# Optimization experiments

Hardware: AMD Instinct MI355X
Metric: run time of the kernel (lower is better)

The kernel has to match this reference:

```python
import jax, jax.numpy as jnp
import numpy as np

EMBED, ACT, MEM, STOCH, HID = 256, 7, 200, 30, 200
MIN_STD = 0.1
T, B = 256, 512


def setup_inputs() -> dict:
    key = jax.random.key(0)
    ks = jax.random.split(key, 16)

    def w(k, shape, fan_in):
        return (jax.random.normal(k, shape, jnp.float32) / np.sqrt(fan_in)).astype(jnp.float32)

    inp = {
        "embed": jax.random.normal(ks[0], (T, B, EMBED), jnp.float32),
        "action": jax.random.normal(ks[1], (T, B, ACT), jnp.float32),
        "reset": jax.random.randint(ks[2], (T, B), 0, 2).astype(bool),
        "in_state": jnp.zeros((B, MEM), jnp.float32),
        "noise": jax.random.normal(ks[3], (B, STOCH), jnp.float32),
        # ea_mlp: Linear(embed+action -> hidden)
        "W_ea": w(ks[4], (EMBED + ACT, HID), EMBED + ACT),
        "b_ea": jnp.zeros((HID,), jnp.float32),
        # GRUCell(hidden -> mem): torch layout [3*mem] ordered (r, z, n)
        "W_ih": w(ks[5], (HID, 3 * MEM), HID),
        "b_ih": jnp.zeros((3 * MEM,), jnp.float32),
        "W_hh": w(ks[6], (MEM, 3 * MEM), MEM),
        "b_hh": jnp.zeros((3 * MEM,), jnp.float32),
        # post_mlp: Linear(mem->hidden), ELU, Linear(hidden->2*stoch)
        "Wp1": w(ks[7], (MEM, HID), MEM),
        "bp1": jnp.zeros((HID,), jnp.float32),
        "Wp2": w(ks[8], (HID, 2 * STOCH), HID),
        "bp2": jnp.zeros((2 * STOCH,), jnp.float32),
    }
    return inp


def reference(embed, action, reset, in_state, noise,
              W_ea, b_ea, W_ih, b_ih, W_hh, b_hh, Wp1, bp1, Wp2, bp2):
    def post_mlp(h):
        mid = jax.nn.elu(h @ Wp1 + bp1)
        return mid @ Wp2 + bp2

    def to_mean_std(x):
        mean, std = jnp.split(x, 2, axis=-1)
        return jnp.concatenate([mean, jax.nn.softplus(std) + MIN_STD], axis=-1)

    def step(h, xs):
        e, a, r = xs  # e:[B,EMBED] a:[B,ACT] r:[B] bool
        h = h * (~r)[:, None].astype(h.dtype)
        ea = jax.nn.elu(jnp.concatenate([e, a], axis=-1) @ W_ea + b_ea)
        gi = ea @ W_ih + b_ih  # [B, 3*MEM]
        gh = h @ W_hh + b_hh
        gi_r, gi_z, gi_n = jnp.split(gi, 3, axis=-1)
        gh_r, gh_z, gh_n = jnp.split(gh, 3, axis=-1)
        rg = jax.nn.sigmoid(gi_r + gh_r)
        zg = jax.nn.sigmoid(gi_z + gh_z)
        ng = jnp.tanh(gi_n + rg * gh_n)
        h_new = (1.0 - zg) * ng + zg * h  # torch GRUCell update
        post = to_mean_std(post_mlp(h_new))
        return h_new, (h_new, post)

    _, (states, posts) = jax.lax.scan(step, in_state, (embed, action, reset))
    mean, std = jnp.split(posts[-1], 2, axis=-1)
    sample = mean + std * noise  # rsample of diag Normal
    return sample, states, posts
```

## Files before the change

kernel.cpp:

```cpp
#include <hip/hip_runtime.h>
#include <math.h>

#define EMBED 256
#define ACTD  7
#define MEM   200
#define STOCH 30
#define T_    256
#define B_    512
#define EAIN  263
#define G3    600

typedef unsigned int uint32;
typedef _Float16 h2v   __attribute__((ext_vector_type(2)));
typedef _Float16 f16x8 __attribute__((ext_vector_type(8)));
typedef float    f32x4 __attribute__((ext_vector_type(4)));

__device__ __forceinline__ float eluf(float x)  { return x > 0.f ? x : expm1f(x); }
__device__ __forceinline__ float sigmf(float x) { return 1.f / (1.f + __expf(-x)); }
__device__ __forceinline__ float splusf(float x){ return fmaxf(x, 0.f) + log1pf(__expf(-fabsf(x))); }

__device__ __forceinline__ uint32 packh2(float a, float b) {
#if __has_builtin(__builtin_amdgcn_cvt_pkrtz)
    auto h = __builtin_amdgcn_cvt_pkrtz(a, b);
    return __builtin_bit_cast(uint32, h);
#else
    h2v h; h.x = (_Float16)a; h.y = (_Float16)b;
    return __builtin_bit_cast(uint32, h);
#endif
}

__global__ void detect_kernel(const unsigned char* __restrict__ p, int n, int* __restrict__ flags)
{
    __shared__ int s_mis, s_gt1;
    if (threadIdx.x == 0) { s_mis = 0; s_gt1 = 0; }
    __syncthreads();
    int mis = 0, gt1 = 0;
    for (int i = threadIdx.x; i < n; i += blockDim.x) {
        unsigned char v = p[i];
        if (v) {
            if (i & 3) mis = 1;
            if (v > 1) gt1 = 1;
        }
    }
    if (mis) atomicOr(&s_mis, 1);
    if (gt1) atomicOr(&s_gt1, 1);
    __syncthreads();
    if (threadIdx.x == 0) flags[0] = s_mis ? (s_gt1 ? 2 : 1) : 0;
}

__device__ __forceinline__ bool resetval(const unsigned char* __restrict__ p, int mode, int idx)
{
    if (mode == 0) return ((const int*)p)[idx] != 0;
    if (mode == 1) return p[idx] != 0;
    return ((const float*)p)[idx] != 0.f;
}

__global__ void packT_kernel(const float* __restrict__ src, uint32* __restrict__ dst,
                             int K, int C, int Cpad, int K2pad)
{
    int idx = blockIdx.x * blockDim.x + threadIdx.x;
    if (idx < Cpad * K2pad) {
        int c = idx / K2pad, k2 = idx % K2pad;
        float a = (c < C && 2 * k2     < K) ? src[(size_t)(2 * k2)     * C + c] : 0.f;
        float b = (c < C && 2 * k2 + 1 < K) ? src[(size_t)(2 * k2 + 1) * C + c] : 0.f;
        dst[idx] = packh2(a, b);
    }
}

#define GI3_T 512

__global__ __launch_bounds__(GI3_T)
void gi3_kernel(const float* __restrict__ embed, const float* __restrict__ action,
                const uint32* __restrict__ WeaT, const float* __restrict__ b_ea,
                const uint32* __restrict__ WihT, const float* __restrict__ b_ih,
                uint32* __restrict__ gi_pk, int row_base)
{
    __shared__ __align__(16) uint32 Epk[32 * 148];
    __shared__ __align__(16) uint32 eapk[32 * 116];

    const int tid = threadIdx.x, lane = tid & 63, wv = tid >> 6;
    const int lo = lane & 15, hi = lane >> 4, r0 = hi * 4;
    const int rel0 = blockIdx.x * 32;
    const int rg0  = row_base + rel0;

    for (int idx = tid; idx < 32 * 144; idx += GI3_T) {
        int r = idx / 144, k2 = idx % 144;
        size_t rg = (size_t)(rg0 + r);
        float a = 0.f, b = 0.f;
        if (k2 < 128) {
            const float2 v = *(const float2*)&embed[rg * EMBED + 2 * k2];
            a = v.x; b = v.y;
        } else if (k2 < 132) {
            int k = 2 * k2 - EMBED;
            a = action[rg * ACTD + k];
            b = (k + 1 < ACTD) ? action[rg * ACTD + k + 1] : 0.f;
        }
        Epk[r * 148 + k2] = packh2(a, b);
    }
    { int r = tid >> 4, o = tid & 15; eapk[r * 116 + 100 + o] = 0; }
    __syncthreads();

    const _Float16* E16  = (const _Float16*)Epk;
    _Float16*       ea16 = (_Float16*)eapk;

    f16x8 afr[2][9];
    #pragma unroll
    for (int mt = 0; mt < 2; mt++)
        #pragma unroll
        for (int kt = 0; kt < 9; kt++)
            afr[mt][kt] = *(const f16x8*)&E16[(mt * 16 + lo) * 296 + kt * 32 + hi * 8];

    for (int nt = wv; nt < 13; nt += 8) {
        int col = nt * 16 + lo;
        float bv = (col < 200) ? b_ea[col] : 0.f;
        f16x8 wb[9];
        #pragma unroll
        for (int kt = 0; kt < 9; kt++)
            wb[kt] = *(const f16x8*)&WeaT[col * 144 + kt * 16 + hi * 4];
        #pragma unroll
        for (int mt = 0; mt < 2; mt++) {
            f32x4 acc = {bv, bv, bv, bv};
            #pragma unroll
            for (int kt = 0; kt < 9; kt++)
                acc = __builtin_amdgcn_mfma_f32_16x16x32_f16(afr[mt][kt], wb[kt], acc, 0, 0, 0);
            #pragma unroll
            for (int j = 0; j < 4; j++)
                ea16[(mt * 16 + r0 + j) * 232 + col] = (_Float16)eluf(acc[j]);
        }
    }
    __syncthreads();

    f16x8 afr2[2][7];
    #pragma unroll
    for (int mt = 0; mt < 2; mt++)
        #pragma unroll
        for (int kt = 0; kt < 7; kt++)
            afr2[mt][kt] = *(const f16x8*)&ea16[(mt * 16 + lo) * 232 + kt * 32 + hi * 8];

    for (int nt = wv; nt < 38; nt += 8) {
        int col = nt * 16 + lo;
        float bv = (col < G3) ? b_ih[col] : 0.f;
        f16x8 wb[7];
        #pragma unroll
        for (int kt = 0; kt < 7; kt++)
            wb[kt] = *(const f16x8*)&WihT[col * 112 + kt * 16 + hi * 4];
        #pragma unroll
        for (int mt = 0; mt < 2; mt++) {
            f32x4 acc = {bv, bv, bv, bv};
            #pragma unroll
            for (int kt = 0; kt < 7; kt++)
                acc = __builtin_amdgcn_mfma_f32_16x16x32_f16(afr2[mt][kt], wb[kt], acc, 0, 0, 0);
            #pragma unroll
            for (int j = 0; j < 4; j++) {
                float v = acc[j];
                float p = __shfl_xor(v, 1);
                if (((lane & 1) == 0) && col < G3)
                    gi_pk[(size_t)(rel0 + mt * 16 + r0 + j) * 300 + (col >> 1)] = packh2(v, p);
            }
        }
    }
}

#define RR 8

__global__ __launch_bounds__(512, 2)
void recur5_kernel(const uint32* __restrict__ gi_pk, const uint32* __restrict__ WhhT,
                   const float* __restrict__ b_hh, const float* __restrict__ in_state,
                   const unsigned char* __restrict__ reset_raw, const int* __restrict__ flags,
                   float* __restrict__ out_states, float* __restrict__ h_buf,
                   int t0, int t1, int first)
{
    __shared__ _Float16 h_lds[16 * 232];
    __shared__ float    gh_lds[RR * 612];
    __shared__ float    rst_lds[RR];

    const int tid = threadIdx.x, lane = tid & 63, wv = tid >> 6;
    const int lo = lane & 15, hi = lane >> 4, r0c = hi * 4;
    const int bg0 = blockIdx.x * RR;
    const int mode = flags[0];
    uint32* h32 = (uint32*)h_lds;

    f16x8 bfr[5][7];
    float bcol[5];
    #pragma unroll
    for (int i = 0; i < 5; ++i) {
        int ct  = wv + 8 * i;
        int col = ct * 16 + lo;
        bcol[i] = (ct < 38 && col < G3) ? b_hh[col] : 0.f;
        #pragma unroll
        for (int kt = 0; kt < 7; ++kt)
            bfr[i][kt] = (ct < 38) ? *(const f16x8*)&WhhT[col * 112 + kt * 16 + hi * 4]
                                   : f16x8{0, 0, 0, 0, 0, 0, 0, 0};
    }

    for (int idx = tid; idx < 1056; idx += 512) {
        int r, o;
        if (idx < 128) { r = idx >> 4; o = 100 + (idx & 15); }
        else { int j = idx - 128; r = 8 + j / 116; o = j % 116; }
        h32[r * 116 + o] = 0;
    }

    float hold[2][2];
    #pragma unroll
    for (int it = 0; it < 2; ++it) {
        int u2 = it * 512 + tid;
        if (u2 < RR * 100) {
            int row = u2 / 100, mp = u2 % 100, m = mp * 2;
            float a, b;
            if (first) {
                const float2 v = *(const float2*)&in_state[(size_t)(bg0 + row) * MEM + m];
                a = v.x; b = v.y;
                if (resetval(reset_raw, mode, bg0 + row)) { a = 0.f; b = 0.f; }
            } else {
                const float2 v = *(const float2*)&h_buf[(size_t)(bg0 + row) * MEM + m];
                a = v.x; b = v.y;
            }
            hold[it][0] = a; hold[it][1] = b;
            h32[row * 116 + mp] = packh2(a, b);
        }
    }
    __syncthreads();

    uint32 pcur[2][3], pnxt[2][3];
    {
        const size_t base32 = (size_t)bg0 * 300;
        #pragma unroll
        for (int it = 0; it < 2; ++it) {
            int u2 = it * 512 + tid;
            if (u2 < RR * 100) {
                int row = u2 / 100, mp = u2 % 100;
                pcur[it][0] = gi_pk[base32 + row * 300 + mp];
                pcur[it][1] = gi_pk[base32 + row * 300 + 100 + mp];
                pcur[it][2] = gi_pk[base32 + row * 300 + 200 + mp];
            }
        }
    }

    for (int t = t0; t < t1; ++t) {
        if (t + 1 < t1) {
            const size_t base32 = ((size_t)(t + 1 - t0) * B_ + bg0) * 300;
            #pragma unroll
            for (int it = 0; it < 2; ++it) {
                int u2 = it * 512 + tid;
                if (u2 < RR * 100) {
                    int row = u2 / 100, mp = u2 % 100;
                    pnxt[it][0] = gi_pk[base32 + row * 300 + mp];
                    pnxt[it][1] = gi_pk[base32 + row * 300 + 100 + mp];
                    pnxt[it][2] = gi_pk[base32 + row * 300 + 200 + mp];
                }
            }
        }

        f16x8 afr[7];
        #pragma unroll
        for (int kt = 0; kt < 7; ++kt)
            afr[kt] = *(const f16x8*)&h_lds[lo * 232 + kt * 32 + hi * 8];

        if (tid < RR) {
            int tt = t + 1;
            rst_lds[tid] = (tt < T_ && resetval(reset_raw, mode, tt * B_ + bg0 + tid)) ? 1.f : 0.f;
        }

        #pragma unroll
        for (int i = 0; i < 5; ++i) {
            int ct = wv + 8 * i;
            if (ct >= 38) break;
            f32x4 acc = {bcol[i], bcol[i], bcol[i], bcol[i]};
            #pragma unroll
            for (int kt = 0; kt < 7; ++kt)
                acc = __builtin_amdgcn_mfma_f32_16x16x32_f16(afr[kt], bfr[i][kt], acc, 0, 0, 0);
            int col = ct * 16 + lo;
            if (col < G3 && r0c < RR) {
                gh_lds[(r0c + 0) * 612 + col] = acc[0];
                gh_lds[(r0c + 1) * 612 + col] = acc[1];
                gh_lds[(r0c + 2) * 612 + col] = acc[2];
                gh_lds[(r0c + 3) * 612 + col] = acc[3];
            }
        }
        __syncthreads();

        #pragma unroll
        for (int it = 0; it < 2; ++it) {
            int u2 = it * 512 + tid;
            if (u2 < RR * 100) {
                int row = u2 / 100, mp = u2 % 100, m = mp * 2;
                h2v g_r = __builtin_bit_cast(h2v, pcur[it][0]);
                h2v g_z = __builtin_bit_cast(h2v, pcur[it][1]);
                h2v g_n = __builtin_bit_cast(h2v, pcur[it][2]);
                const float2 ghr = *(const float2*)&gh_lds[row * 612 + m];
                const float2 ghz = *(const float2*)&gh_lds[row * 612 + 200 + m];
                const float2 ghn = *(const float2*)&gh_lds[row * 612 + 400 + m];
                float hn0, hn1;
                {
                    float rg = sigmf((float)g_r.x + ghr.x);
                    float zg = sigmf((float)g_z.x + ghz.x);
                    float x  = (float)g_n.x + rg * ghn.x;
                    x = fminf(fmaxf(x, -30.f), 30.f);
                    float e2 = __expf(2.f * x);
                    float ng = (e2 - 1.f) / (e2 + 1.f);
                    hn0 = (1.f - zg) * ng + zg * hold[it][0];
                }
                {
                    float rg = sigmf((float)g_r.y + ghr.y);
                    float zg = sigmf((float)g_z.y + ghz.y);
                    float x  = (float)g_n.y + rg * ghn.y;
                    x = fminf(fmaxf(x, -30.f), 30.f);
                    float e2 = __expf(2.f * x);
                    float ng = (e2 - 1.f) / (e2 + 1.f);
                    hn1 = (1.f - zg) * ng + zg * hold[it][1];
                }
                *(float2*)&out_states[((size_t)t * B_ + (bg0 + row)) * MEM + m] = make_float2(hn0, hn1);
                if (rst_lds[row] != 0.f) { hn0 = 0.f; hn1 = 0.f; }
                hold[it][0] = hn0; hold[it][1] = hn1;
                h32[row * 116 + mp] = packh2(hn0, hn1);
            }
        }
        #pragma unroll
        for (int it = 0; it < 2; ++it) {
            pcur[it][0] = pnxt[it][0]; pcur[it][1] = pnxt[it][1]; pcur[it][2] = pnxt[it][2];
        }
        __syncthreads();
    }

    #pragma unroll
    for (int it = 0; it < 2; ++it) {
        int u2 = it * 512 + tid;
        if (u2 < RR * 100) {
            int row = u2 / 100, mp = u2 % 100, m = mp * 2;
            *(float2*)&h_buf[(size_t)(bg0 + row) * MEM + m] = make_float2(hold[it][0], hold[it][1]);
        }
    }
}

__global__ __launch_bounds__(512)
void post3_kernel(const float* __restrict__ states, const uint32* __restrict__ Wp1T,
                  const float* __restrict__ bp1, const uint32* __restrict__ Wp2T,
                  const float* __restrict__ bp2, float* __restrict__ posts)
{
    __shared__ __align__(16) uint32 hp[32 * 116];
    __shared__ __align__(16) uint32 mpk[32 * 116];

    const int tid = threadIdx.x, lane = tid & 63, wv = tid >> 6;
    const int lo = lane & 15, hi = lane >> 4, r0 = hi * 4;
    const size_t rg0 = (size_t)blockIdx.x * 32;

    { int r = tid >> 4, o = tid & 15; hp[r * 116 + 100 + o] = 0; mpk[r * 116 + 100 + o] = 0; }
    for (int idx = tid; idx < 32 * 100; idx += 512) {
        int r = idx / 100, k2 = idx % 100;
        const float2 v = *(const float2*)&states[(rg0 + r) * MEM + 2 * k2];
        hp[r * 116 + k2] = packh2(v.x, v.y);
    }
    __syncthreads();

    const _Float16* h16 = (const _Float16*)hp;
    _Float16*       m16 = (_Float16*)mpk;

    f16x8 afr[2][7];
    #pragma unroll
    for (int mt = 0; mt < 2; mt++)
        #pragma unroll
        for (int kt = 0; kt < 7; kt++)
            afr[mt][kt] = *(const f16x8*)&h16[(mt * 16 + lo) * 232 + kt * 32 + hi * 8];

    for (int nt = wv; nt < 13; nt += 8) {
        int col = nt * 16 + lo;
        float bv = (col < MEM) ? bp1[col] : 0.f;
        f16x8 wb[7];
        #pragma unroll
        for (int kt = 0; kt < 7; kt++)
            wb[kt] = *(const f16x8*)&Wp1T[col * 112 + kt * 16 + hi * 4];
        #pragma unroll
        for (int mt = 0; mt < 2; mt++) {
            f32x4 acc = {bv, bv, bv, bv};
            #pragma unroll
            for (int kt = 0; kt < 7; kt++)
                acc = __builtin_amdgcn_mfma_f32_16x16x32_f16(afr[mt][kt], wb[kt], acc, 0, 0, 0);
            #pragma unroll
            for (int j = 0; j < 4; j++)
                m16[(mt * 16 + r0 + j) * 232 + col] = (_Float16)eluf(acc[j]);
        }
    }
    __syncthreads();

    {
        int nt = wv & 3, mt = wv >> 2;
        int col = nt * 16 + lo;
        float bv = (col < 60) ? bp2[col] : 0.f;
        f16x8 a2[7], wb[7];
        #pragma unroll
        for (int kt = 0; kt < 7; kt++) {
            a2[kt] = *(const f16x8*)&m16[(mt * 16 + lo) * 232 + kt * 32 + hi * 8];
            wb[kt] = *(const f16x8*)&Wp2T[col * 112 + kt * 16 + hi * 4];
        }
        f32x4 acc = {bv, bv, bv, bv};
        #pragma unroll
        for (int kt = 0; kt < 7; kt++)
            acc = __builtin_amdgcn_mfma_f32_16x16x32_f16(a2[kt], wb[kt], acc, 0, 0, 0);
        if (col < 60) {
            #pragma unroll
            for (int j = 0; j < 4; j++) {
                float v = acc[j];
                posts[(rg0 + mt * 16 + r0 + j) * 60 + col] = (col < 30) ? v : (splusf(v) + 0.1f);
            }
        }
    }
}

__global__ void sample_kernel(const float* __restrict__ posts_last,
                              const float* __restrict__ noise, float* __restrict__ out)
{
    int idx = blockIdx.x * blockDim.x + threadIdx.x;
    if (idx < B_ * STOCH) {
        int b = idx / STOCH, s = idx % STOCH;
        float mean = posts_last[b * 60 + s];
        float stdv = posts_last[b * 60 + 30 + s];
        out[idx] = mean + stdv * noise[idx];
    }
}

extern "C" void kernel_launch(void* const* d_in, const int* in_sizes, int n_in,
                              void* d_out, int out_size, void* d_ws, size_t ws_size,
                              hipStream_t stream)
{
    const float* embed   = (const float*)d_in[0];
    const float* action  = (const float*)d_in[1];
    const unsigned char* reset = (const unsigned char*)d_in[2];
    const float* in_state = (const float*)d_in[3];
    const float* noise   = (const float*)d_in[4];
    const float* W_ea = (const float*)d_in[5];
    const float* b_ea = (const float*)d_in[6];
    const float* W_ih = (const float*)d_in[7];
    const float* b_ih = (const float*)d_in[8];
    const float* W_hh = (const float*)d_in[9];
    const float* b_hh = (const float*)d_in[10];
    const float* Wp1  = (const float*)d_in[11];
    const float* bp1  = (const float*)d_in[12];
    const float* Wp2  = (const float*)d_in[13];
    const float* bp2  = (const float*)d_in[14];

    float* out_sample = (float*)d_out;
    float* out_states = out_sample + (size_t)B_ * STOCH;
    float* out_posts  = out_states + (size_t)T_ * B_ * MEM;

    char* ws = (char*)d_ws;
    size_t off = 0;
    int*    flags = (int*)(ws + off);    off += 256;
    float*  h_buf = (float*)(ws + off);  off += (size_t)B_ * MEM * 4;
    uint32* WeaT  = (uint32*)(ws + off); off += (size_t)208 * 144 * 4;
    uint32* WihT  = (uint32*)(ws + off); off += (size_t)608 * 112 * 4;
    uint32* WhhT  = (uint32*)(ws + off); off += (size_t)608 * 112 * 4;
    uint32* Wp1T  = (uint32*)(ws + off); off += (size_t)208 * 112 * 4;
    uint32* Wp2T  = (uint32*)(ws + off); off += (size_t)64 * 112 * 4;
    uint32* gi_buf = (uint32*)(ws + off);

    const size_t per_t = (size_t)B_ * 300 * 4;
    size_t avail = (ws_size > off) ? (ws_size - off) : 0;
    int maxT = (int)(avail / per_t);
    int chunkT = 1;
    while (chunkT * 2 <= maxT && chunkT < T_) chunkT *= 2;

    detect_kernel<<<1, 1024, 0, stream>>>(reset, T_ * B_, flags);
    packT_kernel<<<(208 * 144 + 255) / 256, 256, 0, stream>>>(W_ea, WeaT, EAIN, 200, 208, 144);
    packT_kernel<<<(608 * 112 + 255) / 256, 256, 0, stream>>>(W_ih, WihT, 200, 600, 608, 112);
    packT_kernel<<<(608 * 112 + 255) / 256, 256, 0, stream>>>(W_hh, WhhT, 200, 600, 608, 112);
    packT_kernel<<<(208 * 112 + 255) / 256, 256, 0, stream>>>(Wp1, Wp1T, 200, 200, 208, 112);
    packT_kernel<<<(64 * 112 + 255) / 256, 256, 0, stream>>>(Wp2, Wp2T, 200, 60, 64, 112);

    for (int t0 = 0; t0 < T_; t0 += chunkT) {
        int rows = chunkT * B_;
        gi3_kernel<<<rows / 32, GI3_T, 0, stream>>>(
            embed, action, WeaT, b_ea, WihT, b_ih, gi_buf, t0 * B_);
        recur5_kernel<<<B_ / RR, 512, 0, stream>>>(
            gi_buf, WhhT, b_hh, in_state, reset, flags,
            out_states, h_buf, t0, t0 + chunkT, (t0 == 0) ? 1 : 0);
    }

    post3_kernel<<<(T_ * B_) / 32, 512, 0, stream>>>(
        out_states, Wp1T, bp1, Wp2T, bp2, out_posts);

    sample_kernel<<<(B_ * STOCH + 255) / 256, 256, 0, stream>>>(
        out_posts + (size_t)(T_ - 1) * B_ * 60, noise, out_sample);
}
```

Measured before the change: 920.2 us.

## Interleave GRU gate columns so each wave computes r,z,n in registers

The W_ih/W_hh weights and the precomputed input gates are repacked so that each 16-column group holds matching r, z and n columns for the same hidden units. Each wave in the recurrent kernel now owns whole hidden-unit slices, computes all three gate accumulators and applies the GRU update directly from MFMA registers. This removes the gh shared-memory round trip and one barrier per timestep, and double-buffers the hidden state in LDS. In exchange the wave load is uneven (some waves own one slice, others two), only half the MFMA output rows are used for the 8 batch rows, and the output stores are scalar rather than float2.

```diff
diff --git a/kernel.cpp b/kernel.cpp
--- a/kernel.cpp
+++ b/kernel.cpp
@@ -9,6 +9,8 @@
 #define B_    512
 #define EAIN  263
 #define G3    600
+#define NCP   624
+#define K2P   112
 
 typedef unsigned int uint32;
 typedef _Float16 h2v   __attribute__((ext_vector_type(2)));
@@ -18,6 +20,11 @@
 __device__ __forceinline__ float eluf(float x)  { return x > 0.f ? x : expm1f(x); }
 __device__ __forceinline__ float sigmf(float x) { return 1.f / (1.f + __expf(-x)); }
 __device__ __forceinline__ float splusf(float x){ return fmaxf(x, 0.f) + log1pf(__expf(-fabsf(x))); }
+__device__ __forceinline__ float tanhc(float x) {
+    x = fminf(fmaxf(x, -30.f), 30.f);
+    float e2 = __expf(2.f * x);
+    return (e2 - 1.f) / (e2 + 1.f);
+}
 
 __device__ __forceinline__ uint32 packh2(float a, float b) {
 #if __has_builtin(__builtin_amdgcn_cvt_pkrtz)
@@ -67,13 +74,31 @@
     }
 }
 
+__global__ void packP_kernel(const float* __restrict__ src, uint32* __restrict__ dst)
+{
+    int idx = blockIdx.x * blockDim.x + threadIdx.x;
+    if (idx < NCP * K2P) {
+        int colp = idx / K2P, k2 = idx % K2P;
+        int sg = colp / 48, rem = colp % 48;
+        int g = rem >> 4, i = rem & 15;
+        int m = sg * 16 + i;
+        float a = 0.f, b = 0.f;
+        if (m < 200) {
+            int c = g * 200 + m;
+            if (2 * k2     < 200) a = src[(size_t)(2 * k2)     * G3 + c];
+            if (2 * k2 + 1 < 200) b = src[(size_t)(2 * k2 + 1) * G3 + c];
+        }
+        dst[idx] = packh2(a, b);
+    }
+}
+
 #define GI3_T 512
 
 __global__ __launch_bounds__(GI3_T)
 void gi3_kernel(const float* __restrict__ embed, const float* __restrict__ action,
                 const uint32* __restrict__ WeaT, const float* __restrict__ b_ea,
-                const uint32* __restrict__ WihT, const float* __restrict__ b_ih,
-                uint32* __restrict__ gi_pk, int row_base)
+                const uint32* __restrict__ WihP, const float* __restrict__ b_ih,
+                uint32* __restrict__ gi_pm, int row_base)
 {
     __shared__ __align__(16) uint32 Epk[32 * 148];
     __shared__ __align__(16) uint32 eapk[32 * 116];
@@ -137,197 +162,167 @@
         for (int kt = 0; kt < 7; kt++)
             afr2[mt][kt] = *(const f16x8*)&ea16[(mt * 16 + lo) * 232 + kt * 32 + hi * 8];
 
-    for (int nt = wv; nt < 38; nt += 8) {
-        int col = nt * 16 + lo;
-        float bv = (col < G3) ? b_ih[col] : 0.f;
+    for (int nt = wv; nt < 39; nt += 8) {
+        int colp = nt * 16 + lo;
+        int sg = colp / 48, rem = colp % 48;
+        int g = rem >> 4, i = rem & 15;
+        int m = sg * 16 + i;
+        float bv = (m < 200) ? b_ih[g * 200 + m] : 0.f;
         f16x8 wb[7];
         #pragma unroll
         for (int kt = 0; kt < 7; kt++)
-            wb[kt] = *(const f16x8*)&WihT[col * 112 + kt * 16 + hi * 4];
+            wb[kt] = *(const f16x8*)&WihP[(size_t)colp * K2P + kt * 16 + hi * 4];
         #pragma unroll
         for (int mt = 0; mt < 2; mt++) {
             f32x4 acc = {bv, bv, bv, bv};
             #pragma unroll
             for (int kt = 0; kt < 7; kt++)
                 acc = __builtin_amdgcn_mfma_f32_16x16x32_f16(afr2[mt][kt], wb[kt], acc, 0, 0, 0);
-            #pragma unroll
-            for (int j = 0; j < 4; j++) {
-                float v = acc[j];
-                float p = __shfl_xor(v, 1);
-                if (((lane & 1) == 0) && col < G3)
-                    gi_pk[(size_t)(rel0 + mt * 16 + r0 + j) * 300 + (col >> 1)] = packh2(v, p);
-            }
-        }
-    }
-}
-
-#define RR 8
+            int rp = (rel0 + mt * 16 + r0) >> 1;
+            gi_pm[(size_t)rp       * NCP + colp] = packh2(acc[0], acc[1]);
+            gi_pm[(size_t)(rp + 1) * NCP + colp] = packh2(acc[2], acc[3]);
+        }
+    }
+}
 
 __global__ __launch_bounds__(512, 2)
-void recur5_kernel(const uint32* __restrict__ gi_pk, const uint32* __restrict__ WhhT,
+void recur6_kernel(const uint32* __restrict__ gi_pm, const uint32* __restrict__ WhhP,
                    const float* __restrict__ b_hh, const float* __restrict__ in_state,
                    const unsigned char* __restrict__ reset_raw, const int* __restrict__ flags,
                    float* __restrict__ out_states, float* __restrict__ h_buf,
                    int t0, int t1, int first)
 {
-    __shared__ _Float16 h_lds[16 * 232];
-    __shared__ float    gh_lds[RR * 612];
-    __shared__ float    rst_lds[RR];
+    __shared__ _Float16 hbuf[2][16 * 232];
 
     const int tid = threadIdx.x, lane = tid & 63, wv = tid >> 6;
-    const int lo = lane & 15, hi = lane >> 4, r0c = hi * 4;
-    const int bg0 = blockIdx.x * RR;
+    const int lo = lane & 15, hi = lane >> 4;
+    const int bg0 = blockIdx.x * 8;
     const int mode = flags[0];
-    uint32* h32 = (uint32*)h_lds;
-
-    f16x8 bfr[5][7];
-    float bcol[5];
-    #pragma unroll
-    for (int i = 0; i < 5; ++i) {
-        int ct  = wv + 8 * i;
-        int col = ct * 16 + lo;
-        bcol[i] = (ct < 38 && col < G3) ? b_hh[col] : 0.f;
-        #pragma unroll
-        for (int kt = 0; kt < 7; ++kt)
-            bfr[i][kt] = (ct < 38) ? *(const f16x8*)&WhhT[col * 112 + kt * 16 + hi * 4]
-                                   : f16x8{0, 0, 0, 0, 0, 0, 0, 0};
-    }
-
-    for (int idx = tid; idx < 1056; idx += 512) {
-        int r, o;
-        if (idx < 128) { r = idx >> 4; o = 100 + (idx & 15); }
-        else { int j = idx - 128; r = 8 + j / 116; o = j % 116; }
-        h32[r * 116 + o] = 0;
-    }
-
-    float hold[2][2];
-    #pragma unroll
-    for (int it = 0; it < 2; ++it) {
-        int u2 = it * 512 + tid;
-        if (u2 < RR * 100) {
-            int row = u2 / 100, mp = u2 % 100, m = mp * 2;
-            float a, b;
-            if (first) {
-                const float2 v = *(const float2*)&in_state[(size_t)(bg0 + row) * MEM + m];
-                a = v.x; b = v.y;
-                if (resetval(reset_raw, mode, bg0 + row)) { a = 0.f; b = 0.f; }
-            } else {
-                const float2 v = *(const float2*)&h_buf[(size_t)(bg0 + row) * MEM + m];
-                a = v.x; b = v.y;
-            }
-            hold[it][0] = a; hold[it][1] = b;
-            h32[row * 116 + mp] = packh2(a, b);
-        }
-    }
-    __syncthreads();
-
-    uint32 pcur[2][3], pnxt[2][3];
-    {
-        const size_t base32 = (size_t)bg0 * 300;
-        #pragma unroll
-        for (int it = 0; it < 2; ++it) {
-            int u2 = it * 512 + tid;
-            if (u2 < RR * 100) {
-                int row = u2 / 100, mp = u2 % 100;
-                pcur[it][0] = gi_pk[base32 + row * 300 + mp];
-                pcur[it][1] = gi_pk[base32 + row * 300 + 100 + mp];
-                pcur[it][2] = gi_pk[base32 + row * 300 + 200 + mp];
-            }
-        }
-    }
-
+
+    const int cnt = (wv < 4 || wv == 7) ? 2 : 1;
+    const int sg0 = (wv < 4) ? 2 * wv : wv + 4;
+    const bool act = (hi < 2);
+
+    f16x8 bfr[2][3][7];
+    float bias[2][3];
+    #pragma unroll
+    for (int u = 0; u < 2; ++u) {
+        int sg = sg0 + u;
+        int m = sg * 16 + lo;
+        bool live = (u < cnt);
+        #pragma unroll
+        for (int g = 0; g < 3; ++g) {
+            int colp = sg * 48 + g * 16 + lo;
+            bias[u][g] = (live && m < 200) ? b_hh[g * 200 + m] : 0.f;
+            #pragma unroll
+            for (int kt = 0; kt < 7; ++kt)
+                bfr[u][g][kt] = live ? *(const f16x8*)&WhhP[(size_t)colp * K2P + kt * 16 + hi * 4]
+                                     : f16x8{0, 0, 0, 0, 0, 0, 0, 0};
+        }
+    }
+
+    for (int i = tid; i < 2 * 16 * 116; i += 512) ((uint32*)hbuf)[i] = 0;
+    __syncthreads();
+
+    float hold[2][4];
+    #pragma unroll
+    for (int u = 0; u < 2; ++u) {
+        int sg = sg0 + u, m = sg * 16 + lo;
+        if (act && u < cnt && m < 200) {
+            #pragma unroll
+            for (int j = 0; j < 4; ++j) {
+                int row = hi * 4 + j, bg = bg0 + row;
+                float h;
+                if (first) {
+                    h = in_state[(size_t)bg * MEM + m];
+                    if (resetval(reset_raw, mode, bg)) h = 0.f;
+                } else {
+                    h = h_buf[(size_t)bg * MEM + m];
+                }
+                hold[u][j] = h;
+                hbuf[0][row * 232 + m] = (_Float16)h;
+            }
+        }
+    }
+    __syncthreads();
+
+    int p = 0;
     for (int t = t0; t < t1; ++t) {
-        if (t + 1 < t1) {
-            const size_t base32 = ((size_t)(t + 1 - t0) * B_ + bg0) * 300;
-            #pragma unroll
-            for (int it = 0; it < 2; ++it) {
-                int u2 = it * 512 + tid;
-                if (u2 < RR * 100) {
-                    int row = u2 / 100, mp = u2 % 100;
-                    pnxt[it][0] = gi_pk[base32 + row * 300 + mp];
-                    pnxt[it][1] = gi_pk[base32 + row * 300 + 100 + mp];
-                    pnxt[it][2] = gi_pk[base32 + row * 300 + 200 + mp];
+        uint32 pcur[2][3][2];
+        bool rnext[4];
+        const size_t rpb = ((size_t)(t - t0) * B_ + bg0) >> 1;
+        if (act) {
+            #pragma unroll
+            for (int u = 0; u < 2; ++u) {
+                int sg = sg0 + u;
+                #pragma unroll
+                for (int g = 0; g < 3; ++g)
+                    #pragma unroll
+                    for (int jp = 0; jp < 2; ++jp)
+                        pcur[u][g][jp] = (u < cnt)
+                            ? gi_pm[(rpb + hi * 2 + jp) * NCP + sg * 48 + g * 16 + lo] : 0u;
+            }
+            #pragma unroll
+            for (int j = 0; j < 4; ++j) {
+                int tt = t + 1;
+                rnext[j] = (tt < T_) && resetval(reset_raw, mode, tt * B_ + bg0 + hi * 4 + j);
+            }
+        }
+
+        f32x4 acc[2][3];
+        #pragma unroll
+        for (int u = 0; u < 2; ++u)
+            #pragma unroll
+            for (int g = 0; g < 3; ++g)
+                acc[u][g] = f32x4{bias[u][g], bias[u][g], bias[u][g], bias[u][g]};
+        #pragma unroll
+        for (int kt = 0; kt < 7; ++kt) {
+            f16x8 a = *(const f16x8*)&hbuf[p][lo * 232 + kt * 32 + hi * 8];
+            #pragma unroll
+            for (int u = 0; u < 2; ++u) {
+                if (u < cnt) {
+                    #pragma unroll
+                    for (int g = 0; g < 3; ++g)
+                        acc[u][g] = __builtin_amdgcn_mfma_f32_16x16x32_f16(a, bfr[u][g][kt], acc[u][g], 0, 0, 0);
                 }
             }
         }
 
-        f16x8 afr[7];
-        #pragma unroll
-        for (int kt = 0; kt < 7; ++kt)
-            afr[kt] = *(const f16x8*)&h_lds[lo * 232 + kt * 32 + hi * 8];
-
-        if (tid < RR) {
-            int tt = t + 1;
-            rst_lds[tid] = (tt < T_ && resetval(reset_raw, mode, tt * B_ + bg0 + tid)) ? 1.f : 0.f;
-        }
-
-        #pragma unroll
-        for (int i = 0; i < 5; ++i) {
-            int ct = wv + 8 * i;
-            if (ct >= 38) break;
-            f32x4 acc = {bcol[i], bcol[i], bcol[i], bcol[i]};
-            #pragma unroll
-            for (int kt = 0; kt < 7; ++kt)
-                acc = __builtin_amdgcn_mfma_f32_16x16x32_f16(afr[kt], bfr[i][kt], acc, 0, 0, 0);
-            int col = ct * 16 + lo;
-            if (col < G3 && r0c < RR) {
-                gh_lds[(r0c + 0) * 612 + col] = acc[0];
-                gh_lds[(r0c + 1) * 612 + col] = acc[1];
-                gh_lds[(r0c + 2) * 612 + col] = acc[2];
-                gh_lds[(r0c + 3) * 612 + col] = acc[3];
+        #pragma unroll
+        for (int u = 0; u < 2; ++u) {
+            int sg = sg0 + u, m = sg * 16 + lo;
+            if (act && u < cnt && m < 200) {
+                #pragma unroll
+                for (int j = 0; j < 4; ++j) {
+                    int row = hi * 4 + j;
+                    h2v g_r = __builtin_bit_cast(h2v, pcur[u][0][j >> 1]);
+                    h2v g_z = __builtin_bit_cast(h2v, pcur[u][1][j >> 1]);
+                    h2v g_n = __builtin_bit_cast(h2v, pcur[u][2][j >> 1]);
+                    float gir = (j & 1) ? (float)g_r.y : (float)g_r.x;
+                    float giz = (j & 1) ? (float)g_z.y : (float)g_z.x;
+                    float gin = (j & 1) ? (float)g_n.y : (float)g_n.x;
+                    float rg = sigmf(gir + acc[u][0][j]);
+                    float zg = sigmf(giz + acc[u][1][j]);
+                    float ng = tanhc(gin + rg * acc[u][2][j]);
+                    float hn = (1.f - zg) * ng + zg * hold[u][j];
+                    out_states[((size_t)t * B_ + bg0 + row) * MEM + m] = hn;
+                    if (rnext[j]) hn = 0.f;
+                    hold[u][j] = hn;
+                    hbuf[p ^ 1][row * 232 + m] = (_Float16)hn;
+                }
             }
         }
         __syncthreads();
-
-        #pragma unroll
-        for (int it = 0; it < 2; ++it) {
-            int u2 = it * 512 + tid;
-            if (u2 < RR * 100) {
-                int row = u2 / 100, mp = u2 % 100, m = mp * 2;
-                h2v g_r = __builtin_bit_cast(h2v, pcur[it][0]);
-                h2v g_z = __builtin_bit_cast(h2v, pcur[it][1]);
-                h2v g_n = __builtin_bit_cast(h2v, pcur[it][2]);
-                const float2 ghr = *(const float2*)&gh_lds[row * 612 + m];
-                const float2 ghz = *(const float2*)&gh_lds[row * 612 + 200 + m];
-                const float2 ghn = *(const float2*)&gh_lds[row * 612 + 400 + m];
-                float hn0, hn1;
-                {
-                    float rg = sigmf((float)g_r.x + ghr.x);
-                    float zg = sigmf((float)g_z.x + ghz.x);
-                    float x  = (float)g_n.x + rg * ghn.x;
-                    x = fminf(fmaxf(x, -30.f), 30.f);
-                    float e2 = __expf(2.f * x);
-                    float ng = (e2 - 1.f) / (e2 + 1.f);
-                    hn0 = (1.f - zg) * ng + zg * hold[it][0];
-                }
-                {
-                    float rg = sigmf((float)g_r.y + ghr.y);
-                    float zg = sigmf((float)g_z.y + ghz.y);
-                    float x  = (float)g_n.y + rg * ghn.y;
-                    x = fminf(fmaxf(x, -30.f), 30.f);
-                    float e2 = __expf(2.f * x);
-                    float ng = (e2 - 1.f) / (e2 + 1.f);
-                    hn1 = (1.f - zg) * ng + zg * hold[it][1];
-                }
-                *(float2*)&out_states[((size_t)t * B_ + (bg0 + row)) * MEM + m] = make_float2(hn0, hn1);
-                if (rst_lds[row] != 0.f) { hn0 = 0.f; hn1 = 0.f; }
-                hold[it][0] = hn0; hold[it][1] = hn1;
-                h32[row * 116 + mp] = packh2(hn0, hn1);
-            }
-        }
-        #pragma unroll
-        for (int it = 0; it < 2; ++it) {
-            pcur[it][0] = pnxt[it][0]; pcur[it][1] = pnxt[it][1]; pcur[it][2] = pnxt[it][2];
-        }
-        __syncthreads();
-    }
-
-    #pragma unroll
-    for (int it = 0; it < 2; ++it) {
-        int u2 = it * 512 + tid;
-        if (u2 < RR * 100) {
-            int row = u2 / 100, mp = u2 % 100, m = mp * 2;
-            *(float2*)&h_buf[(size_t)(bg0 + row) * MEM + m] = make_float2(hold[it][0], hold[it][1]);
+        p ^= 1;
+    }
+
+    #pragma unroll
+    for (int u = 0; u < 2; ++u) {
+        int sg = sg0 + u, m = sg * 16 + lo;
+        if (act && u < cnt && m < 200) {
+            #pragma unroll
+            for (int j = 0; j < 4; ++j)
+                h_buf[(size_t)(bg0 + hi * 4 + j) * MEM + m] = hold[u][j];
         }
     }
 }
@@ -447,13 +442,13 @@
     int*    flags = (int*)(ws + off);    off += 256;
     float*  h_buf = (float*)(ws + off);  off += (size_t)B_ * MEM * 4;
     uint32* WeaT  = (uint32*)(ws + off); off += (size_t)208 * 144 * 4;
-    uint32* WihT  = (uint32*)(ws + off); off += (size_t)608 * 112 * 4;
-    uint32* WhhT  = (uint32*)(ws + off); off += (size_t)608 * 112 * 4;
+    uint32* WihP  = (uint32*)(ws + off); off += (size_t)NCP * K2P * 4;
+    uint32* WhhP  = (uint32*)(ws + off); off += (size_t)NCP * K2P * 4;
     uint32* Wp1T  = (uint32*)(ws + off); off += (size_t)208 * 112 * 4;
     uint32* Wp2T  = (uint32*)(ws + off); off += (size_t)64 * 112 * 4;
-    uint32* gi_buf = (uint32*)(ws + off);
-
-    const size_t per_t = (size_t)B_ * 300 * 4;
+    uint32* gi_pm = (uint32*)(ws + off);
+
+    const size_t per_t = (size_t)(B_ / 2) * NCP * 4;
     size_t avail = (ws_size > off) ? (ws_size - off) : 0;
     int maxT = (int)(avail / per_t);
     int chunkT = 1;
@@ -461,17 +456,17 @@
 
     detect_kernel<<<1, 1024, 0, stream>>>(reset, T_ * B_, flags);
     packT_kernel<<<(208 * 144 + 255) / 256, 256, 0, stream>>>(W_ea, WeaT, EAIN, 200, 208, 144);
-    packT_kernel<<<(608 * 112 + 255) / 256, 256, 0, stream>>>(W_ih, WihT, 200, 600, 608, 112);
-    packT_kernel<<<(608 * 112 + 255) / 256, 256, 0, stream>>>(W_hh, WhhT, 200, 600, 608, 112);
+    packP_kernel<<<(NCP * K2P + 255) / 256, 256, 0, stream>>>(W_ih, WihP);
+    packP_kernel<<<(NCP * K2P + 255) / 256, 256, 0, stream>>>(W_hh, WhhP);
     packT_kernel<<<(208 * 112 + 255) / 256, 256, 0, stream>>>(Wp1, Wp1T, 200, 200, 208, 112);
     packT_kernel<<<(64 * 112 + 255) / 256, 256, 0, stream>>>(Wp2, Wp2T, 200, 60, 64, 112);
 
     for (int t0 = 0; t0 < T_; t0 += chunkT) {
         int rows = chunkT * B_;
         gi3_kernel<<<rows / 32, GI3_T, 0, stream>>>(
-            embed, action, WeaT, b_ea, WihT, b_ih, gi_buf, t0 * B_);
-        recur5_kernel<<<B_ / RR, 512, 0, stream>>>(
-            gi_buf, WhhT, b_hh, in_state, reset, flags,
+            embed, action, WeaT, b_ea, WihP, b_ih, gi_pm, t0 * B_);
+        recur6_kernel<<<B_ / 8, 512, 0, stream>>>(
+            gi_pm, WhhP, b_hh, in_state, reset, flags,
             out_states, h_buf, t0, t0 + chunkT, (t0 == 0) ? 1 : 0);
     }
 
```

New measurement: 1.342 ms. +45.8%, slower.

## Halve batch rows per recurrence block to double block count

Applied to the files above, without the earlier changes.

Reduces the batch rows handled by each recurrent GRU block from 8 to 4, which launches twice as many blocks (128 instead of 64) across the GPU's compute units. Each thread now handles at most one element pair per step, so the two-iteration elementwise loops collapse to a single guarded path. The gh scratch stride is padded to 624. Every block still loads the full W_hh fragments and runs the same 16-row MFMAs, so redundant weight and MFMA work per row doubles.

```diff
diff --git a/kernel.cpp b/kernel.cpp
--- a/kernel.cpp
+++ b/kernel.cpp
@@ -9,6 +9,7 @@
 #define B_    512
 #define EAIN  263
 #define G3    600
+#define GHSTR 624
 
 typedef unsigned int uint32;
 typedef _Float16 h2v   __attribute__((ext_vector_type(2)));
@@ -161,17 +162,17 @@
     }
 }
 
-#define RR 8
+#define RR 4
 
 __global__ __launch_bounds__(512, 2)
-void recur5_kernel(const uint32* __restrict__ gi_pk, const uint32* __restrict__ WhhT,
+void recur9_kernel(const uint32* __restrict__ gi_pk, const uint32* __restrict__ WhhT,
                    const float* __restrict__ b_hh, const float* __restrict__ in_state,
                    const unsigned char* __restrict__ reset_raw, const int* __restrict__ flags,
                    float* __restrict__ out_states, float* __restrict__ h_buf,
                    int t0, int t1, int first)
 {
     __shared__ _Float16 h_lds[16 * 232];
-    __shared__ float    gh_lds[RR * 612];
+    __shared__ float    gh_lds[RR * GHSTR];
     __shared__ float    rst_lds[RR];
 
     const int tid = threadIdx.x, lane = tid & 63, wv = tid >> 6;
@@ -193,62 +194,47 @@
                                    : f16x8{0, 0, 0, 0, 0, 0, 0, 0};
     }
 
-    for (int idx = tid; idx < 1056; idx += 512) {
+    for (int idx = tid; idx < 1456; idx += 512) {
         int r, o;
-        if (idx < 128) { r = idx >> 4; o = 100 + (idx & 15); }
-        else { int j = idx - 128; r = 8 + j / 116; o = j % 116; }
+        if (idx < 64) { r = idx >> 4; o = 100 + (idx & 15); }
+        else { int j = idx - 64; r = RR + j / 116; o = j % 116; }
         h32[r * 116 + o] = 0;
     }
 
-    float hold[2][2];
-    #pragma unroll
-    for (int it = 0; it < 2; ++it) {
-        int u2 = it * 512 + tid;
-        if (u2 < RR * 100) {
-            int row = u2 / 100, mp = u2 % 100, m = mp * 2;
-            float a, b;
-            if (first) {
-                const float2 v = *(const float2*)&in_state[(size_t)(bg0 + row) * MEM + m];
-                a = v.x; b = v.y;
-                if (resetval(reset_raw, mode, bg0 + row)) { a = 0.f; b = 0.f; }
-            } else {
-                const float2 v = *(const float2*)&h_buf[(size_t)(bg0 + row) * MEM + m];
-                a = v.x; b = v.y;
-            }
-            hold[it][0] = a; hold[it][1] = b;
-            h32[row * 116 + mp] = packh2(a, b);
-        }
-    }
-    __syncthreads();
-
-    uint32 pcur[2][3], pnxt[2][3];
-    {
-        const size_t base32 = (size_t)bg0 * 300;
-        #pragma unroll
-        for (int it = 0; it < 2; ++it) {
-            int u2 = it * 512 + tid;
-            if (u2 < RR * 100) {
-                int row = u2 / 100, mp = u2 % 100;
-                pcur[it][0] = gi_pk[base32 + row * 300 + mp];
-                pcur[it][1] = gi_pk[base32 + row * 300 + 100 + mp];
-                pcur[it][2] = gi_pk[base32 + row * 300 + 200 + mp];
-            }
-        }
+    const bool gact = (tid < RR * 100);
+    const int  grow = tid / 100, gmp = tid % 100, gm = gmp * 2;
+    const int  gbg  = bg0 + grow;
+
+    float hold0 = 0.f, hold1 = 0.f;
+    if (gact) {
+        float a, b;
+        if (first) {
+            const float2 v = *(const float2*)&in_state[(size_t)gbg * MEM + gm];
+            a = v.x; b = v.y;
+            if (resetval(reset_raw, mode, gbg)) { a = 0.f; b = 0.f; }
+        } else {
+            const float2 v = *(const float2*)&h_buf[(size_t)gbg * MEM + gm];
+            a = v.x; b = v.y;
+        }
+        hold0 = a; hold1 = b;
+        h32[grow * 116 + gmp] = packh2(a, b);
+    }
+    __syncthreads();
+
+    uint32 pcur[3], pnxt[3];
+    if (gact) {
+        const size_t base = ((size_t)gbg) * 300;
+        pcur[0] = gi_pk[base + gmp];
+        pcur[1] = gi_pk[base + 100 + gmp];
+        pcur[2] = gi_pk[base + 200 + gmp];
     }
 
     for (int t = t0; t < t1; ++t) {
-        if (t + 1 < t1) {
-            const size_t base32 = ((size_t)(t + 1 - t0) * B_ + bg0) * 300;
-            #pragma unroll
-            for (int it = 0; it < 2; ++it) {
-                int u2 = it * 512 + tid;
-                if (u2 < RR * 100) {
-                    int row = u2 / 100, mp = u2 % 100;
-                    pnxt[it][0] = gi_pk[base32 + row * 300 + mp];
-                    pnxt[it][1] = gi_pk[base32 + row * 300 + 100 + mp];
-                    pnxt[it][2] = gi_pk[base32 + row * 300 + 200 + mp];
-                }
-            }
+        if (gact && t + 1 < t1) {
+            const size_t base = ((size_t)(t + 1 - t0) * B_ + gbg) * 300;
+            pnxt[0] = gi_pk[base + gmp];
+            pnxt[1] = gi_pk[base + 100 + gmp];
+            pnxt[2] = gi_pk[base + 200 + gmp];
         }
 
         f16x8 afr[7];
@@ -271,65 +257,51 @@
                 acc = __builtin_amdgcn_mfma_f32_16x16x32_f16(afr[kt], bfr[i][kt], acc, 0, 0, 0);
             int col = ct * 16 + lo;
             if (col < G3 && r0c < RR) {
-                gh_lds[(r0c + 0) * 612 + col] = acc[0];
-                gh_lds[(r0c + 1) * 612 + col] = acc[1];
-                gh_lds[(r0c + 2) * 612 + col] = acc[2];
-                gh_lds[(r0c + 3) * 612 + col] = acc[3];
+                gh_lds[(r0c + 0) * GHSTR + col] = acc[0];
+                gh_lds[(r0c + 1) * GHSTR + col] = acc[1];
+                gh_lds[(r0c + 2) * GHSTR + col] = acc[2];
+                gh_lds[(r0c + 3) * GHSTR + col] = acc[3];
             }
         }
         __syncthreads();
 
-        #pragma unroll
-        for (int it = 0; it < 2; ++it) {
-            int u2 = it * 512 + tid;
-            if (u2 < RR * 100) {
-                int row = u2 / 100, mp = u2 % 100, m = mp * 2;
-                h2v g_r = __builtin_bit_cast(h2v, pcur[it][0]);
-                h2v g_z = __builtin_bit_cast(h2v, pcur[it][1]);
-                h2v g_n = __builtin_bit_cast(h2v, pcur[it][2]);
-                const float2 ghr = *(const float2*)&gh_lds[row * 612 + m];
-                const float2 ghz = *(const float2*)&gh_lds[row * 612 + 200 + m];
-                const float2 ghn = *(const float2*)&gh_lds[row * 612 + 400 + m];
-                float hn0, hn1;
-                {
-                    float rg = sigmf((float)g_r.x + ghr.x);
-                    float zg = sigmf((float)g_z.x + ghz.x);
-                    float x  = (float)g_n.x + rg * ghn.x;
-                    x = fminf(fmaxf(x, -30.f), 30.f);
-                    float e2 = __expf(2.f * x);
-                    float ng = (e2 - 1.f) / (e2 + 1.f);
-                    hn0 = (1.f - zg) * ng + zg * hold[it][0];
-                }
-                {
-                    float rg = sigmf((float)g_r.y + ghr.y);
-                    float zg = sigmf((float)g_z.y + ghz.y);
-                    float x  = (float)g_n.y + rg * ghn.y;
-                    x = fminf(fmaxf(x, -30.f), 30.f);
-                    float e2 = __expf(2.f * x);
-                    float ng = (e2 - 1.f) / (e2 + 1.f);
-                    hn1 = (1.f - zg) * ng + zg * hold[it][1];
-                }
-                *(float2*)&out_states[((size_t)t * B_ + (bg0 + row)) * MEM + m] = make_float2(hn0, hn1);
-                if (rst_lds[row] != 0.f) { hn0 = 0.f; hn1 = 0.f; }
-                hold[it][0] = hn0; hold[it][1] = hn1;
-                h32[row * 116 + mp] = packh2(hn0, hn1);
+        if (gact) {
+            h2v g_r = __builtin_bit_cast(h2v, pcur[0]);
+            h2v g_z = __builtin_bit_cast(h2v, pcur[1]);
+            h2v g_n = __builtin_bit_cast(h2v, pcur[2]);
+            const float2 ghr = *(const float2*)&gh_lds[grow * GHSTR + gm];
+            const float2 ghz = *(const float2*)&gh_lds[grow * GHSTR + 200 + gm];
+            const float2 ghn = *(const float2*)&gh_lds[grow * GHSTR + 400 + gm];
+            float hn0, hn1;
+            {
+                float rg = sigmf((float)g_r.x + ghr.x);
+                float zg = sigmf((float)g_z.x + ghz.x);
+                float x  = (float)g_n.x + rg * ghn.x;
+                x = fminf(fmaxf(x, -30.f), 30.f);
+                float e2 = __expf(2.f * x);
+                float ng = (e2 - 1.f) / (e2 + 1.f);
+                hn0 = (1.f - zg) * ng + zg * hold0;
             }
-        }
-        #pragma unroll
-        for (int it = 0; it < 2; ++it) {
-            pcur[it][0] = pnxt[it][0]; pcur[it][1] = pnxt[it][1]; pcur[it][2] = pnxt[it][2];
-        }
+            {
+                float rg = sigmf((float)g_r.y + ghr.y);
+                float zg = sigmf((float)g_z.y + ghz.y);
+                float x  = (float)g_n.y + rg * ghn.y;
+                x = fminf(fmaxf(x, -30.f), 30.f);
+                float e2 = __expf(2.f * x);
+                float ng = (e2 - 1.f) / (e2 + 1.f);
+                hn1 = (1.f - zg) * ng + zg * hold1;
+            }
+            *(float2*)&out_states[((size_t)t * B_ + gbg) * MEM + gm] = make_float2(hn0, hn1);
+            if (rst_lds[grow] != 0.f) { hn0 = 0.f; hn1 = 0.f; }
+            hold0 = hn0; hold1 = hn1;
+            h32[grow * 116 + gmp] = packh2(hn0, hn1);
+        }
+        pcur[0] = pnxt[0]; pcur[1] = pnxt[1]; pcur[2] = pnxt[2];
         __syncthreads();
     }
 
-    #pragma unroll
-    for (int it = 0; it < 2; ++it) {
-        int u2 = it * 512 + tid;
-        if (u2 < RR * 100) {
-            int row = u2 / 100, mp = u2 % 100, m = mp * 2;
-            *(float2*)&h_buf[(size_t)(bg0 + row) * MEM + m] = make_float2(hold[it][0], hold[it][1]);
-        }
-    }
+    if (gact)
+        *(float2*)&h_buf[(size_t)gbg * MEM + gm] = make_float2(hold0, hold1);
 }
 
 __global__ __launch_bounds__(512)
@@ -470,7 +442,7 @@
         int rows = chunkT * B_;
         gi3_kernel<<<rows / 32, GI3_T, 0, stream>>>(
             embed, action, WeaT, b_ea, WihT, b_ih, gi_buf, t0 * B_);
-        recur5_kernel<<<B_ / RR, 512, 0, stream>>>(
+        recur9_kernel<<<B_ / RR, 512, 0, stream>>>(
             gi_buf, WhhT, b_hh, in_state, reset, flags,
             out_states, h_buf, t0, t0 + chunkT, (t0 == 0) ? 1 : 0);
     }
```

Result: faster. 796.0 us (-13.5%).
